# Optimization experiments

Hardware: AMD Instinct MI355X
Metric: run time of the kernel (lower is better)

## Reference

```python
import jax, jax.numpy as jnp
import numpy as np

DX, DZ, DT = 10.0, 10.0, 1.0e-3
NX, NZ = 512, 512
NSTEPS, NREC = 512, 128
DT2 = DT * DT
INV_DXDZ = 1.0 / (DX * DZ)


def setup_inputs() -> dict:
    key = jax.random.key(0)
    k1, k2, k3, k4 = jax.random.split(key, 4)
    # velocity in [1500, 2500] m/s -> CFL stable with dt=1e-3, dx=dz=10
    velocity_model = 1500.0 + 1000.0 * jax.random.uniform(k1, (NX, NZ), dtype=jnp.float32)
    source = jax.random.normal(k2, (NSTEPS,), dtype=jnp.float32)
    rec_x = jax.random.randint(k3, (NREC,), 0, NX)
    rec_z = jax.random.randint(k4, (NREC,), 0, NZ)
    return {
        "velocity_model": velocity_model,
        "source": source,
        "src_x": 256,
        "src_z": 8,
        "rec_x": rec_x,
        "rec_z": rec_z,
    }


def _laplacian(p):
    # 3x3 cross stencil with zero padding, scaled by 1/(dx*dz) -- identical to
    # F.conv2d(p, [[0,1,0],[1,-4,1],[0,1,0]]/(dx*dz), padding=1)
    pp = jnp.pad(p, 1)
    return (pp[:-2, 1:-1] + pp[2:, 1:-1] + pp[1:-1, :-2] + pp[1:-1, 2:] - 4.0 * p) * INV_DXDZ


def reference(velocity_model, source, src_x, src_z, rec_x, rec_z):
    v2_dt2 = velocity_model * velocity_model * DT2  # [nx, nz]

    def step(carry, s_t):
        p, p_old = carry
        p_new = 2.0 * p - p_old + v2_dt2 * _laplacian(p)
        p_new = p_new.at[src_x, src_z].add(s_t * DT2)
        return (p_new, p), p_new[rec_x, rec_z]  # gather all receivers at once

    p0 = jnp.zeros((NX, NZ), dtype=velocity_model.dtype)
    _, recs = jax.lax.scan(step, (p0, p0), source)  # recs: [n_steps, n_rec]
    return recs.T  # seismogram: [n_rec, n_steps]
```

## Files before the change

### kernel.cpp

```cpp
#include <hip/hip_runtime.h>


#define NXd 512
#define NZd 512
#define NSTEPSd 512
#define NRECd 128
#define DT2f 1.0e-6f
#define INVf 1.0e-2f
#define TBk 16
#define TIk 32
#define EXTk 64
#define NTILEk 16
#define PADk 16
#define PWk 544
#define LROWS 66
#define NROUNDS (NSTEPSd / TBk)

__device__ __forceinline__ float dpp_shr1(float x) {
    int v = __builtin_amdgcn_update_dpp(0, __builtin_bit_cast(int, x),
                                        0x138, 0xF, 0xF, false);
    return __builtin_bit_cast(float, v);
}
__device__ __forceinline__ float dpp_shl1(float x) {
    int v = __builtin_amdgcn_update_dpp(0, __builtin_bit_cast(int, x),
                                        0x130, 0xF, 0xF, false);
    return __builtin_bit_cast(float, v);
}

__device__ __forceinline__ float2 ldg_f2(const float2* p) {
    unsigned long long v = __hip_atomic_load(
        (const unsigned long long*)p, __ATOMIC_RELAXED, __HIP_MEMORY_SCOPE_AGENT);
    return __builtin_bit_cast(float2, v);
}
__device__ __forceinline__ float ldg_f1(const float* p) {
    unsigned v = __hip_atomic_load(
        (const unsigned*)p, __ATOMIC_RELAXED, __HIP_MEMORY_SCOPE_AGENT);
    return __builtin_bit_cast(float, v);
}
__device__ __forceinline__ void stg_f2(float2* p, float2 x) {
    __hip_atomic_store((unsigned long long*)p,
                       __builtin_bit_cast(unsigned long long, x),
                       __ATOMIC_RELAXED, __HIP_MEMORY_SCOPE_AGENT);
}

__global__ __launch_bounds__(1024) void fdtd_persist(
    const float* __restrict__ vel, const float* __restrict__ source,
    const int* __restrict__ src_x, const int* __restrict__ src_z,
    const int* __restrict__ rec_x, const int* __restrict__ rec_z,
    float2* __restrict__ PA, float2* __restrict__ PB,
    float* __restrict__ out, unsigned* __restrict__ done)
{
    __shared__ float sb[2][LROWS * EXTk];

    const int tid = threadIdx.x;
    const int w   = tid >> 6;
    const int ez  = tid & 63;
    const int bx = blockIdx.x, by = blockIdx.y;
    const int gx0 = by * TIk;
    const int gz0 = bx * TIk;
    const int ox = gx0 - TBk, oz = gz0 - TBk;
    const int myid = (by * NTILEk + bx) * 32;

    for (int i = tid; i < 34 * 34; i += 1024) {
        const int p = (by * 34 + i / 34) * PWk + (bx * 34 + i % 34);
        stg_f2(&PA[p], make_float2(0.f, 0.f));
        stg_f2(&PB[p], make_float2(0.f, 0.f));
    }

    bool rOwn = false; int rIdx = 0;
    if (tid < NRECd) {
        const int rx = rec_x[tid], rz = rec_z[tid];
        rOwn = (rx >= gx0 && rx < gx0 + TIk && rz >= gz0 && rz < gz0 + TIk);
        rIdx = (rx - ox + 1) * EXTk + (rz - oz);
        if (rOwn) {
            float4* o4 = (float4*)&out[tid * NSTEPSd];
            #pragma unroll
            for (int j = 0; j < NSTEPSd / 4; ++j) o4[j] = make_float4(0.f, 0.f, 0.f, 0.f);
        }
    }

    float rV2i[4];
    {
        const int fz = oz + ez;
        #pragma unroll
        for (int i = 0; i < 4; ++i) {
            const int fx = ox + 4 * w + i;
            float v2 = 0.f;
            if (fx >= 0 && fx < NXd && fz >= 0 && fz < NZd) {
                float v = vel[fx * NZd + fz];
                v2 = v * v * (DT2f * INVf);
            }
            rV2i[i] = v2;
        }
    }

    if (w == 0) {
        sb[0][ez] = 0.f;
        sb[0][(LROWS - 1) * EXTk + ez] = 0.f;
        sb[1][ez] = 0.f;
        sb[1][(LROWS - 1) * EXTk + ez] = 0.f;
    }

    const int sx = *src_x, sz = *src_z;
    const int exs = sx - ox, ezs = sz - oz;
    const bool srcHere = (exs >= 0 && exs < EXTk && ezs >= 0 && ezs < EXTk) &&
                         (tid == (((exs >> 2) << 6) | ezs));

    const int dxm = max(0, max(ox - sx, sx - (ox + EXTk - 1)));
    const int dzm = max(0, max(oz - sz, sz - (oz + EXTk - 1)));
    const int dman = dxm + dzm;
    const int kAct = dman <= (TBk + 1) ? 0 : (dman - (TBk + 1) + TBk - 1) / TBk;

    const int lane = tid & 63;
    int nb = myid;
    if (lane < 8) {
        const int d = (lane < 4) ? lane : lane + 1;
        const int ny = min(NTILEk - 1, max(0, by + d / 3 - 1));
        const int nx = min(NTILEk - 1, max(0, bx + d % 3 - 1));
        nb = (ny * NTILEk + nx) * 32;
    }

    const int pbase = (gx0 + 4 * w) * PWk + gz0 + ez;
    const int fbase = 4 * w * EXTk + ez;

    __syncthreads();
    if (tid == 0)
        __hip_atomic_store(&done[myid], (unsigned)(kAct + 1),
                           __ATOMIC_RELAXED, __HIP_MEMORY_SCOPE_AGENT);

    for (int k = kAct; k < NROUNDS; ++k) {
        const int t0 = TBk * k;

        if (lane < 8) {
            const unsigned tgt = (unsigned)(k + 1);
            for (;;) {
                unsigned seen = __hip_atomic_load(&done[nb], __ATOMIC_RELAXED,
                                                  __HIP_MEMORY_SCOPE_AGENT);
                if (seen >= tgt) break;
                if (seen + 1 < tgt) __builtin_amdgcn_s_sleep(16);
                else                __builtin_amdgcn_s_sleep(1);
            }
        }

        float2* __restrict__ Pin  = (k & 1) ? PB : PA;
        float2* __restrict__ Pout = (k & 1) ? PA : PB;

        float2 co[4];
        #pragma unroll
        for (int i = 0; i < 4; ++i) co[i] = ldg_f2(&Pin[pbase + i * PWk]);
        const float huG = ldg_f1((const float*)&Pin[pbase - PWk]);
        const float hdG = ldg_f1((const float*)&Pin[pbase + 4 * PWk]);

        float rCur[4], rOld[4];
        #pragma unroll
        for (int i = 0; i < 4; ++i) { rCur[i] = co[i].x; rOld[i] = co[i].y; }

        float sv[TBk];
        if (srcHere) {
            #pragma unroll
            for (int s = 0; s < TBk; ++s) sv[s] = source[t0 + s] * DT2f;
        }

        float rv[TBk];
        #pragma unroll
        for (int s = 0; s < TBk; ++s) {
            const float* cur = sb[s & 1];
            float* nxt = sb[(s & 1) ^ 1];
            const float up0 = (s == 0) ? huG : cur[fbase];
            const float dn3 = (s == 0) ? hdG : cur[fbase + 5 * EXTk];
            float nv[4];
            #pragma unroll
            for (int i = 0; i < 4; ++i) {
                const float up = (i == 0) ? up0 : rCur[i - 1];
                const float dn = (i == 3) ? dn3 : rCur[i + 1];
                const float lf = dpp_shr1(rCur[i]);
                const float rt = dpp_shl1(rCur[i]);
                const float sum = (up + dn) + (lf + rt);
                const float t4 = __builtin_fmaf(-4.0f, rCur[i], sum);
                const float pm = __builtin_fmaf(2.0f, rCur[i], -rOld[i]);
                nv[i] = __builtin_fmaf(rV2i[i], t4, pm);
            }
            #pragma unroll
            for (int i = 0; i < 4; ++i) {
                rOld[i] = rCur[i];
                rCur[i] = nv[i];
                nxt[fbase + (1 + i) * EXTk] = nv[i];
            }
            if (srcHere) {
                #pragma unroll
                for (int i = 0; i < 4; ++i) {
                    if (i == (exs & 3)) {
                        rCur[i] += sv[s];
                        nxt[(exs + 1) * EXTk + ezs] = rCur[i];
                    }
                }
            }
            __syncthreads();
            if (rOwn) rv[s] = nxt[rIdx];
        }

        if (w >= 4 && w < 12 && ez >= TBk && ez < EXTk - TBk) {
            #pragma unroll
            for (int i = 0; i < 4; ++i)
                stg_f2(&Pout[pbase + i * PWk], make_float2(rCur[i], rOld[i]));
        }

        __syncthreads();
        if (tid == 0)
            __hip_atomic_store(&done[myid], (unsigned)(k + 2),
                               __ATOMIC_RELAXED, __HIP_MEMORY_SCOPE_AGENT);

        if (rOwn) {
            #pragma unroll
            for (int s = 0; s < TBk; ++s)
                out[tid * NSTEPSd + t0 + s] = rv[s];
        }
    }
}

extern "C" void kernel_launch(void* const* d_in, const int* in_sizes, int n_in,
                              void* d_out, int out_size, void* d_ws, size_t ws_size,
                              hipStream_t stream) {
    const float* vel    = (const float*)d_in[0];
    const float* source = (const float*)d_in[1];
    const int*   src_x  = (const int*)d_in[2];
    const int*   src_z  = (const int*)d_in[3];
    const int*   rec_x  = (const int*)d_in[4];
    const int*   rec_z  = (const int*)d_in[5];
    float* out = (float*)d_out;

    const size_t FP = (size_t)PWk * PWk;
    float2* base = (float2*)d_ws;
    float2* PA = base + PWk;
    float2* PB = PA + FP;
    unsigned* DONE = (unsigned*)(PB + FP + PWk);

    hipMemsetAsync(DONE, 0, (size_t)NTILEk * NTILEk * 32 * sizeof(unsigned), stream);

    void* args[] = {(void*)&vel, (void*)&source, (void*)&src_x, (void*)&src_z,
                    (void*)&rec_x, (void*)&rec_z, (void*)&PA, (void*)&PB,
                    (void*)&out, (void*)&DONE};
    hipLaunchCooperativeKernel((void*)fdtd_persist, dim3(NTILEk, NTILEk),
                               dim3(1024), args, 0, stream);
}
```

Baseline: 340.4 us.

## Replace per-substep block barriers with neighbor-wave LDS flag synchronization

Result: slower. 392.1 us (+15.2%).

```diff
diff --git a/kernel.cpp b/kernel.cpp
--- a/kernel.cpp
+++ b/kernel.cpp
@@ -15,6 +15,7 @@
 #define PWk 544
 #define LROWS 66
 #define NROUNDS (NSTEPSd / TBk)
+#define MAXR 8
 
 __device__ __forceinline__ float dpp_shr1(float x) {
     int v = __builtin_amdgcn_update_dpp(0, __builtin_bit_cast(int, x),
@@ -51,6 +52,7 @@
     float* __restrict__ out, unsigned* __restrict__ done)
 {
     __shared__ float sb[2][LROWS * EXTk];
+    __shared__ int wflag[16 * 16];
 
     const int tid = threadIdx.x;
     const int w   = tid >> 6;
@@ -67,16 +69,17 @@
         stg_f2(&PB[p], make_float2(0.f, 0.f));
     }
 
-    bool rOwn = false; int rIdx = 0;
-    if (tid < NRECd) {
-        const int rx = rec_x[tid], rz = rec_z[tid];
-        rOwn = (rx >= gx0 && rx < gx0 + TIk && rz >= gz0 && rz < gz0 + TIk);
-        rIdx = (rx - ox + 1) * EXTk + (rz - oz);
-        if (rOwn) {
-            float4* o4 = (float4*)&out[tid * NSTEPSd];
-            #pragma unroll
-            for (int j = 0; j < NSTEPSd / 4; ++j) o4[j] = make_float4(0.f, 0.f, 0.f, 0.f);
-        }
+    int nR = 0; int rSlot[MAXR]; int rReg[MAXR];
+    for (int r = 0; r < NRECd; ++r) {
+        const int er = rec_x[r] - ox, ec = rec_z[r] - oz;
+        if (er >= TBk && er < TBk + TIk && ec >= TBk && ec < TBk + TIk &&
+            ec == ez && (er >> 2) == w && nR < MAXR) {
+            rSlot[nR] = r; rReg[nR] = er & 3; ++nR;
+        }
+    }
+    for (int j = 0; j < nR; ++j) {
+        float4* o4 = (float4*)&out[rSlot[j] * NSTEPSd];
+        for (int q = 0; q < NSTEPSd / 4; ++q) o4[q] = make_float4(0.f, 0.f, 0.f, 0.f);
     }
 
     float rV2i[4];
@@ -100,6 +103,7 @@
         sb[1][ez] = 0.f;
         sb[1][(LROWS - 1) * EXTk + ez] = 0.f;
     }
+    if (ez == 0) wflag[w * 16] = 0;
 
     const int sx = *src_x, sz = *src_z;
     const int exs = sx - ox, ezs = sz - oz;
@@ -127,6 +131,8 @@
     if (tid == 0)
         __hip_atomic_store(&done[myid], (unsigned)(kAct + 1),
                            __ATOMIC_RELAXED, __HIP_MEMORY_SCOPE_AGENT);
+
+    int base = 0;
 
     for (int k = kAct; k < NROUNDS; ++k) {
         const int t0 = TBk * k;
@@ -161,9 +167,21 @@
             for (int s = 0; s < TBk; ++s) sv[s] = source[t0 + s] * DT2f;
         }
 
-        float rv[TBk];
         #pragma unroll
         for (int s = 0; s < TBk; ++s) {
+            if (s > 0) {
+                const int tgt = base + s;
+                if (w > 0)
+                    while (__hip_atomic_load(&wflag[(w - 1) * 16],
+                                             __ATOMIC_ACQUIRE,
+                                             __HIP_MEMORY_SCOPE_WORKGROUP) < tgt)
+                        __builtin_amdgcn_s_sleep(1);
+                if (w < 15)
+                    while (__hip_atomic_load(&wflag[(w + 1) * 16],
+                                             __ATOMIC_ACQUIRE,
+                                             __HIP_MEMORY_SCOPE_WORKGROUP) < tgt)
+                        __builtin_amdgcn_s_sleep(1);
+            }
             const float* cur = sb[s & 1];
             float* nxt = sb[(s & 1) ^ 1];
             const float up0 = (s == 0) ? huG : cur[fbase];
@@ -195,9 +213,20 @@
                     }
                 }
             }
-            __syncthreads();
-            if (rOwn) rv[s] = nxt[rIdx];
-        }
+            if (ez == 0)
+                __hip_atomic_store(&wflag[w * 16], base + s + 1,
+                                   __ATOMIC_RELEASE, __HIP_MEMORY_SCOPE_WORKGROUP);
+            #pragma unroll
+            for (int j = 0; j < MAXR; ++j) {
+                if (j < nR) {
+                    const int rr = rReg[j];
+                    const float v = rr == 0 ? rCur[0] : rr == 1 ? rCur[1]
+                                  : rr == 2 ? rCur[2] : rCur[3];
+                    out[rSlot[j] * NSTEPSd + t0 + s] = v;
+                }
+            }
+        }
+        base += TBk;
 
         if (w >= 4 && w < 12 && ez >= TBk && ez < EXTk - TBk) {
             #pragma unroll
@@ -209,12 +238,6 @@
         if (tid == 0)
             __hip_atomic_store(&done[myid], (unsigned)(k + 2),
                                __ATOMIC_RELAXED, __HIP_MEMORY_SCOPE_AGENT);
-
-        if (rOwn) {
-            #pragma unroll
-            for (int s = 0; s < TBk; ++s)
-                out[tid * NSTEPSd + t0 + s] = rv[s];
-        }
     }
 }
 
```
